# Performance work log

Hardware: AMD Instinct MI355X
Metric: run time of the kernel (lower is better)

## Reference

```python
import jax, jax.numpy as jnp
import numpy as np

D = 120000   # sample_size
H1 = 600     # sample_size/200
H2 = 300     # sample_size/400
H3 = 200     # sample_size/600
DENSITY = 0.1  # sparselinear default connectivity
B = 512
EPS = 1e-5

_LAYER_SPECS = [(H1, D), (H1, H1), (H2, H1), (H3, H2), (H3, H3)]


def _make_idx(key, out_d, in_d, nnz):
    k1, k2 = jax.random.split(key)
    rows = jax.random.randint(k1, (nnz,), 0, out_d)
    cols = jax.random.randint(k2, (nnz,), 0, in_d)
    return jnp.stack([rows, cols]).astype(jnp.int32)


def setup_inputs() -> dict:
    key = jax.random.key(0)
    ks = jax.random.split(key, 32)
    inp = {"x": jax.random.normal(ks[0], (B, D), jnp.float32)}
    for i, (o, ii) in enumerate(_LAYER_SPECS, 1):
        nnz = int(DENSITY * o * ii)
        scale = 1.0 / np.sqrt(DENSITY * ii)  # kaiming-like fan-in scaling on nonzeros
        inp[f"idx{i}"] = _make_idx(ks[3 * i], o, ii, nnz)
        inp[f"val{i}"] = jax.random.normal(ks[3 * i + 1], (nnz,), jnp.float32) * scale
        inp[f"b{i}"] = jnp.zeros((o,), jnp.float32)
    for j, d in enumerate([H1, H2, H3], 1):
        inp[f"g{j}"] = jnp.ones((d,), jnp.float32)
        inp[f"be{j}"] = jnp.zeros((d,), jnp.float32)
    return inp


def _sp_linear(x, idx, vals, bias, out_d):
    # COO sparse linear: y = x @ W^T + b, W scattered from (row, col, val)
    in_d = x.shape[1]
    W = jnp.zeros((out_d, in_d), x.dtype).at[idx[0], idx[1]].add(vals)
    return x @ W.T + bias


def _bn(x, g, b):
    # BatchNorm1d, training mode: biased batch variance
    m = x.mean(axis=0)
    v = x.var(axis=0)
    return (x - m) * jax.lax.rsqrt(v + EPS) * g + b


def reference(x, idx1, val1, b1, idx2, val2, b2, idx3, val3, b3,
              idx4, val4, b4, idx5, val5, b5,
              g1, be1, g2, be2, g3, be3):
    h = jax.nn.silu(_bn(_sp_linear(x, idx1, val1, b1, H1), g1, be1))
    h = jax.nn.silu(_sp_linear(h, idx2, val2, b2, H1))
    h = jax.nn.silu(_bn(_sp_linear(h, idx3, val3, b3, H2), g2, be2))
    h = jax.nn.silu(_bn(_sp_linear(h, idx4, val4, b4, H3), g3, be3))
    return _sp_linear(h, idx5, val5, b5, H3)
```

## Files before the change

kernel.cpp:

```cpp
#include <hip/hip_runtime.h>

typedef unsigned short ushort_t;
typedef unsigned int uint_t;

typedef __bf16 bf16x8 __attribute__((ext_vector_type(8)));
typedef float  floatx4 __attribute__((ext_vector_type(4)));

#define AS3 __attribute__((address_space(3)))
#define AS1 __attribute__((address_space(1)))

#define BATCH 512
#define D_IN  120000
#define N1P   640
#define N2P   640
#define N3P   320
#define N4P   256
#define N5P   256

#define KSPLIT 50
#define KCHUNK 2400

#define HALF    60000
#define CHW     15000
#define NREG    1200
#define NB      256
#define RSTRIDE 6912

static constexpr long O_W1 = 0;
static constexpr long SZ_W1 = 640L * 120000 * 2;
static constexpr long O_W2 = O_W1 + SZ_W1;
static constexpr long SZ_W2 = 640L * 640 * 4;
static constexpr long O_W3 = O_W2 + SZ_W2;
static constexpr long SZ_W3 = 320L * 640 * 4;
static constexpr long O_W4 = O_W3 + SZ_W3;
static constexpr long SZ_W4 = 256L * 320 * 4;
static constexpr long O_W5 = O_W4 + SZ_W4;
static constexpr long SZ_W5 = 256L * 256 * 4;
static constexpr long O_Y1 = O_W5 + SZ_W5;
static constexpr long SZ_Y1 = 512L * 640 * 4;
static constexpr long ZERO_OFF = O_W2;
static constexpr long ZERO_BYTES = (O_Y1 + SZ_Y1) - O_W2;
static constexpr long O_XB = O_Y1 + SZ_Y1;
static constexpr long SZ_XB = 512L * 120000 * 2;
static constexpr long O_CNT = O_XB;
static constexpr long O_OFF = O_CNT + (long)NREG * NB * 4;
static constexpr long O_TOT = O_OFF + (long)NB * NREG * 4;
static constexpr long O_REC = O_TOT + 4800;
static constexpr long O_H1 = O_XB;
static constexpr long O_H2 = O_H1 + 512L * 640 * 4;
static constexpr long O_Y3 = O_H2 + 512L * 640 * 4;
static constexpr long O_H3 = O_Y3 + 512L * 320 * 4;
static constexpr long O_Y4 = O_H3 + 512L * 320 * 4;
static constexpr long O_H4 = O_Y4 + 512L * 256 * 4;

__device__ __forceinline__ ushort_t f2bf(float f) {
    union { float f; uint_t u; } x;
    x.f = f;
    uint_t u = x.u;
    return (ushort_t)((u + 0x7FFFu + ((u >> 16) & 1u)) >> 16);
}
__device__ __forceinline__ float silu_f(float z) {
    return z / (1.f + expf(-z));
}
__device__ __forceinline__ void load16_lds(const void* g, void* l) {
    __builtin_amdgcn_global_load_lds((const AS1 char*)g, (AS3 char*)l, 16, 0, 0);
}

__global__ void zero_f4(float4* __restrict__ p, long n4) {
    long stride = (long)gridDim.x * blockDim.x;
    for (long i = (long)blockIdx.x * blockDim.x + threadIdx.x; i < n4; i += stride)
        p[i] = make_float4(0.f, 0.f, 0.f, 0.f);
}

__global__ void cast_f32_bf16(const float* __restrict__ X, ushort_t* __restrict__ Xb, long n8) {
    long t = (long)blockIdx.x * blockDim.x + threadIdx.x;
    if (t >= n8) return;
    const float4* p = (const float4*)X + 2 * t;
    float4 a = p[0], b = p[1];
    union { ushort_t us[8]; uint4 v; } u;
    u.us[0] = f2bf(a.x); u.us[1] = f2bf(a.y); u.us[2] = f2bf(a.z); u.us[3] = f2bf(a.w);
    u.us[4] = f2bf(b.x); u.us[5] = f2bf(b.y); u.us[6] = f2bf(b.z); u.us[7] = f2bf(b.w);
    ((uint4*)Xb)[t] = u.v;
}

__global__ __launch_bounds__(512) void hist1(const int* __restrict__ idx, int nnz, int chunk,
                                             int* __restrict__ counts ) {
    __shared__ uint_t h[NREG];
    const int b = blockIdx.x, t = threadIdx.x;
    for (int i = t; i < NREG; i += 512) h[i] = 0;
    __syncthreads();
    const int s = b * chunk;
    const int e = min(s + chunk, nnz);
    for (int i = s + t; i < e; i += 512) {
        int r = idx[i];
        int c = idx[nnz + i];
        atomicAdd(&h[r * 2 + (c >= HALF ? 1 : 0)], 1u);
    }
    __syncthreads();
    for (int i = t; i < NREG; i += 512) counts[(long)i * NB + b] = (int)h[i];
}

__global__ __launch_bounds__(NB) void scan1(const int* __restrict__ counts ,
                                            int* __restrict__ offs ,
                                            int* __restrict__ totals) {
    __shared__ int s[NB];
    const int reg = blockIdx.x, t = threadIdx.x;
    const int v = counts[(long)reg * NB + t];
    s[t] = v;
    __syncthreads();
    for (int o = 1; o < NB; o <<= 1) {
        int x = (t >= o) ? s[t - o] : 0;
        __syncthreads();
        s[t] += x;
        __syncthreads();
    }
    offs[(long)t * NREG + reg] = s[t] - v;
    if (t == NB - 1) totals[reg] = s[t];
}

__global__ __launch_bounds__(512) void scatter1(const int* __restrict__ idx,
                                                const float* __restrict__ vals,
                                                int nnz, int chunk,
                                                const int* __restrict__ offs ,
                                                int2* __restrict__ rec) {
    __shared__ int cur[NREG];
    const int b = blockIdx.x, t = threadIdx.x;
    const int* ob = offs + (long)b * NREG;
    for (int i = t; i < NREG; i += 512) cur[i] = i * RSTRIDE + ob[i];
    __syncthreads();
    const int s = b * chunk;
    const int e = min(s + chunk, nnz);
    for (int i = s + t; i < e; i += 512) {
        int r = idx[i];
        int c = idx[nnz + i];
        float v = vals[i];
        int h = (c >= HALF) ? 1 : 0;
        int reg = r * 2 + h;
        int slot = atomicAdd(&cur[reg], 1);
        if (slot < (reg + 1) * RSTRIDE)
            rec[slot] = make_int2(c - h * HALF, __float_as_int(v));
    }
}

__global__ __launch_bounds__(512) void build_w1(const int2* __restrict__ rec,
                                                const int* __restrict__ totals,
                                                ushort_t* __restrict__ W) {
    const int bid = blockIdx.x;
    const int r = bid >> 1, h = bid & 1;
    const int t = threadIdx.x;
    ushort_t* dstbase = W + (size_t)r * D_IN + h * HALF;

    if (r >= 600) {
        uint4 z = make_uint4(0, 0, 0, 0);
        for (int j = t * 8; j < HALF; j += 512 * 8) *(uint4*)(dstbase + j) = z;
        return;
    }

    __shared__ int2 lrec[RSTRIDE];
    __shared__ float acc[CHW];

    const int reg = r * 2 + h;
    const int n = min(totals[reg], RSTRIDE);
    const int2* src = rec + (long)reg * RSTRIDE;
    for (int i = t; i < n; i += 512) lrec[i] = src[i];
    __syncthreads();

#pragma unroll
    for (int ch = 0; ch < 4; ch++) {
        for (int j = t * 4; j < CHW; j += 512 * 4)
            *(float4*)&acc[j] = make_float4(0.f, 0.f, 0.f, 0.f);
        __syncthreads();
        const int base = ch * CHW;
        for (int i = t; i < n; i += 512) {
            int2 e = lrec[i];
            unsigned off = (unsigned)(e.x - base);
            if (off < (unsigned)CHW)
                atomicAdd(&acc[off], __int_as_float(e.y));
        }
        __syncthreads();
        ushort_t* dst = dstbase + base;
        for (int j = t * 8; j < CHW; j += 512 * 8) {
            union { ushort_t us[8]; uint4 v; } u;
#pragma unroll
            for (int k = 0; k < 8; k++) u.us[k] = f2bf(acc[j + k]);
            *(uint4*)(dst + j) = u.v;
        }
        __syncthreads();
    }
}

__global__ void scatter_f32(const int* __restrict__ idx, const float* __restrict__ vals,
                            int nnz, float* __restrict__ W, int ldw) {
    int i = blockIdx.x * blockDim.x + threadIdx.x;
    if (i >= nnz) return;
    atomicAdd(&W[(size_t)idx[i] * ldw + idx[nnz + i]], vals[i]);
}

__global__ __launch_bounds__(256) void gemm1(const ushort_t* __restrict__ X,
                                             const ushort_t* __restrict__ W,
                                             float* __restrict__ Y) {
    __shared__ ushort_t sA[2][128 * 32];
    __shared__ ushort_t sB[2][128 * 32];

    const int b = blockIdx.x;
    const int wrk = (b & 7) * 125 + (b >> 3);
    const int ksIdx = wrk / 20;
    const int tile = wrk % 20;
    const int bm = tile / 5, bn = tile % 5;
    const int ks = ksIdx * KCHUNK;
    const int iters = KCHUNK / 32;

    const int t = threadIdx.x;
    const int lane = t & 63;
    const int w = t >> 6;
    const int wm = w >> 1, wn = w & 1;
    const int i16 = lane & 15;
    const int qk = lane >> 4;

    const int row0 = t >> 2;
    const int kq = (t & 3) ^ ((t >> 3) & 3);

    const ushort_t* pa0 = X + (size_t)(bm * 128 + row0) * D_IN + ks + kq * 8;
    const ushort_t* pa1 = pa0 + (size_t)64 * D_IN;
    const ushort_t* pb0 = W + (size_t)(bn * 128 + row0) * D_IN + ks + kq * 8;
    const ushort_t* pb1 = pb0 + (size_t)64 * D_IN;

    int aoff[4], boff[4];
#pragma unroll
    for (int mi = 0; mi < 4; mi++) {
        int row = wm * 64 + mi * 16 + i16;
        aoff[mi] = row * 64 + ((qk ^ ((row >> 1) & 3)) * 16);
    }
#pragma unroll
    for (int ni = 0; ni < 4; ni++) {
        int row = wn * 64 + ni * 16 + i16;
        boff[ni] = row * 64 + ((qk ^ ((row >> 1) & 3)) * 16);
    }
    const char* sAb = (const char*)sA;
    const char* sBb = (const char*)sB;

    floatx4 acc[4][4] = {};

    load16_lds(pa0, &sA[0][(w * 64) * 8]);
    load16_lds(pa1, &sA[0][(256 + w * 64) * 8]);
    load16_lds(pb0, &sB[0][(w * 64) * 8]);
    load16_lds(pb1, &sB[0][(256 + w * 64) * 8]);
    pa0 += 32; pa1 += 32; pb0 += 32; pb1 += 32;
    __syncthreads();

    int cur = 0;
    for (int it = 0; it < iters; ++it) {
        const int nxt = cur ^ 1;
        if (it + 1 < iters) {
            load16_lds(pa0, &sA[nxt][(w * 64) * 8]);
            load16_lds(pa1, &sA[nxt][(256 + w * 64) * 8]);
            load16_lds(pb0, &sB[nxt][(w * 64) * 8]);
            load16_lds(pb1, &sB[nxt][(256 + w * 64) * 8]);
            pa0 += 32; pa1 += 32; pb0 += 32; pb1 += 32;
        }

        bf16x8 af[4], bfr[4];
#pragma unroll
        for (int mi = 0; mi < 4; mi++)
            af[mi] = *(const bf16x8*)(sAb + cur * 8192 + aoff[mi]);
#pragma unroll
        for (int ni = 0; ni < 4; ni++)
            bfr[ni] = *(const bf16x8*)(sBb + cur * 8192 + boff[ni]);
#pragma unroll
        for (int mi = 0; mi < 4; mi++)
#pragma unroll
            for (int ni = 0; ni < 4; ni++)
                acc[mi][ni] = __builtin_amdgcn_mfma_f32_16x16x32_bf16(af[mi], bfr[ni], acc[mi][ni], 0, 0, 0);

        __syncthreads();
        cur = nxt;
    }

#pragma unroll
    for (int mi = 0; mi < 4; mi++) {
#pragma unroll
        for (int ni = 0; ni < 4; ni++) {
#pragma unroll
            for (int r = 0; r < 4; r++) {
                int row = bm * 128 + wm * 64 + mi * 16 + qk * 4 + r;
                int col = bn * 128 + wn * 64 + ni * 16 + i16;
                atomicAdd(&Y[(size_t)row * N1P + col], acc[mi][ni][r]);
            }
        }
    }
}

__global__ __launch_bounds__(512) void bn_silu(const float* __restrict__ Y, int ld, int realN,
                                               const float* __restrict__ g,
                                               const float* __restrict__ be,
                                               float* __restrict__ H) {
    const int t = threadIdx.x;
    const int sub = t >> 6;
    const int c = t & 63;
    const int col = blockIdx.x * 64 + c;

    float s = 0.f, ss = 0.f;
#pragma unroll 8
    for (int r = sub; r < BATCH; r += 8) {
        float v = Y[(size_t)r * ld + col];
        s += v;
        ss += v * v;
    }
    __shared__ float rs[8][64], rq[8][64], scs[64], shs[64];
    rs[sub][c] = s;
    rq[sub][c] = ss;
    __syncthreads();
    if (t < 64) {
        float S = 0.f, SS = 0.f;
#pragma unroll
        for (int k = 0; k < 8; k++) { S += rs[k][t]; SS += rq[k][t]; }
        float mean = S * (1.f / 512.f);
        float var  = SS * (1.f / 512.f) - mean * mean;
        int cc = blockIdx.x * 64 + t;
        float sc = 0.f, sh = 0.f;
        if (cc < realN) {
            sc = rsqrtf(var + 1e-5f) * g[cc];
            sh = be[cc] - mean * sc;
        }
        scs[t] = sc;
        shs[t] = sh;
    }
    __syncthreads();
    const float sc = scs[c], sh = shs[c];
#pragma unroll 8
    for (int r = sub; r < BATCH; r += 8) {
        float v = Y[(size_t)r * ld + col];
        H[(size_t)r * ld + col] = silu_f(v * sc + sh);
    }
}

template <int ACT, int GUARD>
__global__ __launch_bounds__(256) void small_gemm(const float* __restrict__ A, int lda,
                                                  const float* __restrict__ W, int ldw,
                                                  const float* __restrict__ bias, int biasN,
                                                  float* __restrict__ out, int ldo, int outN,
                                                  int K) {
    __shared__ float sA[64][20];
    __shared__ float sB[64][20];
    const int t = threadIdx.x;
    const int m0 = blockIdx.x * 64, n0 = blockIdx.y * 64;
    const int ty = t >> 4, tx = t & 15;
    const int lm = t >> 2, lq = t & 3;
    float acc[4][4] = {};

    for (int kt = 0; kt < K; kt += 16) {
        __syncthreads();
        float4 av = *(const float4*)&A[(size_t)(m0 + lm) * lda + kt + lq * 4];
        float4 wv = *(const float4*)&W[(size_t)(n0 + lm) * ldw + kt + lq * 4];
        sA[lm][lq * 4 + 0] = av.x; sA[lm][lq * 4 + 1] = av.y;
        sA[lm][lq * 4 + 2] = av.z; sA[lm][lq * 4 + 3] = av.w;
        sB[lm][lq * 4 + 0] = wv.x; sB[lm][lq * 4 + 1] = wv.y;
        sB[lm][lq * 4 + 2] = wv.z; sB[lm][lq * 4 + 3] = wv.w;
        __syncthreads();
#pragma unroll
        for (int kg = 0; kg < 4; kg++) {
            float4 a4[4], b4[4];
#pragma unroll
            for (int i = 0; i < 4; i++) a4[i] = *(const float4*)&sA[ty * 4 + i][kg * 4];
#pragma unroll
            for (int j = 0; j < 4; j++) b4[j] = *(const float4*)&sB[tx * 4 + j][kg * 4];
#pragma unroll
            for (int i = 0; i < 4; i++)
#pragma unroll
                for (int j = 0; j < 4; j++)
                    acc[i][j] += a4[i].x * b4[j].x + a4[i].y * b4[j].y +
                                 a4[i].z * b4[j].z + a4[i].w * b4[j].w;
        }
    }

#pragma unroll
    for (int i = 0; i < 4; i++) {
#pragma unroll
        for (int j = 0; j < 4; j++) {
            int row = m0 + ty * 4 + i;
            int col = n0 + tx * 4 + j;
            float v = acc[i][j];
            if (bias != nullptr && col < biasN) v += bias[col];
            if (ACT == 1) v = silu_f(v);
            if (GUARD) {
                if (col < outN) out[(size_t)row * ldo + col] = v;
            } else {
                out[(size_t)row * ldo + col] = v;
            }
        }
    }
}

extern "C" void kernel_launch(void* const* d_in, const int* in_sizes, int n_in,
                              void* d_out, int out_size, void* d_ws, size_t ws_size,
                              hipStream_t stream) {
    const float* x   = (const float*)d_in[0];
    const int* idx1 = (const int*)d_in[1];  const float* val1 = (const float*)d_in[2];
    const int* idx2 = (const int*)d_in[4];  const float* val2 = (const float*)d_in[5];
    const float* b2 = (const float*)d_in[6];
    const int* idx3 = (const int*)d_in[7];  const float* val3 = (const float*)d_in[8];
    const int* idx4 = (const int*)d_in[10]; const float* val4 = (const float*)d_in[11];
    const int* idx5 = (const int*)d_in[13]; const float* val5 = (const float*)d_in[14];
    const float* b5 = (const float*)d_in[15];
    const float* g1 = (const float*)d_in[16]; const float* be1 = (const float*)d_in[17];
    const float* g2 = (const float*)d_in[18]; const float* be2 = (const float*)d_in[19];
    const float* g3 = (const float*)d_in[20]; const float* be3 = (const float*)d_in[21];

    const int nnz1 = in_sizes[1] / 2;
    const int nnz2 = in_sizes[4] / 2;
    const int nnz3 = in_sizes[7] / 2;
    const int nnz4 = in_sizes[10] / 2;
    const int nnz5 = in_sizes[13] / 2;

    char* ws = (char*)d_ws;
    ushort_t* W1 = (ushort_t*)(ws + O_W1);
    float* W2 = (float*)(ws + O_W2);
    float* W3 = (float*)(ws + O_W3);
    float* W4 = (float*)(ws + O_W4);
    float* W5 = (float*)(ws + O_W5);
    float* y1 = (float*)(ws + O_Y1);
    int*   cnt = (int*)(ws + O_CNT);
    int*   off = (int*)(ws + O_OFF);
    int*   tot = (int*)(ws + O_TOT);
    int2*  rec = (int2*)(ws + O_REC);
    ushort_t* Xb = (ushort_t*)(ws + O_XB);
    float* h1 = (float*)(ws + O_H1);
    float* h2 = (float*)(ws + O_H2);
    float* y3 = (float*)(ws + O_Y3);
    float* h3 = (float*)(ws + O_H3);
    float* y4 = (float*)(ws + O_Y4);
    float* h4 = (float*)(ws + O_H4);

    zero_f4<<<dim3((unsigned)(ZERO_BYTES / 16 / 256 + 1)), dim3(256), 0, stream>>>(
        (float4*)(ws + ZERO_OFF), ZERO_BYTES / 16);

    {
        const int chunk = (nnz1 + NB - 1) / NB;
        hist1<<<dim3(NB), dim3(512), 0, stream>>>(idx1, nnz1, chunk, cnt);
        scan1<<<dim3(NREG), dim3(NB), 0, stream>>>(cnt, off, tot);
        scatter1<<<dim3(NB), dim3(512), 0, stream>>>(idx1, val1, nnz1, chunk, off, rec);
        build_w1<<<dim3(640 * 2), dim3(512), 0, stream>>>(rec, tot, W1);
    }

    {
        long n8 = (long)BATCH * D_IN / 8;
        cast_f32_bf16<<<dim3((unsigned)((n8 + 255) / 256)), dim3(256), 0, stream>>>(x, Xb, n8);
    }

    scatter_f32<<<dim3((nnz2 + 255) / 256), dim3(256), 0, stream>>>(idx2, val2, nnz2, W2, 640);
    scatter_f32<<<dim3((nnz3 + 255) / 256), dim3(256), 0, stream>>>(idx3, val3, nnz3, W3, 640);
    scatter_f32<<<dim3((nnz4 + 255) / 256), dim3(256), 0, stream>>>(idx4, val4, nnz4, W4, 320);
    scatter_f32<<<dim3((nnz5 + 255) / 256), dim3(256), 0, stream>>>(idx5, val5, nnz5, W5, 256);

    gemm1<<<dim3(8 * 125), dim3(256), 0, stream>>>(Xb, W1, y1);

    bn_silu<<<dim3(N1P / 64), dim3(512), 0, stream>>>(y1, N1P, 600, g1, be1, h1);

    small_gemm<1, 0><<<dim3(8, N2P / 64), dim3(256), 0, stream>>>(h1, N1P, W2, 640, b2, 600,
                                                                  h2, N2P, N2P, 640);
    small_gemm<0, 0><<<dim3(8, N3P / 64), dim3(256), 0, stream>>>(h2, N2P, W3, 640, nullptr, 0,
                                                                  y3, N3P, N3P, 640);
    bn_silu<<<dim3(N3P / 64), dim3(512), 0, stream>>>(y3, N3P, 300, g2, be2, h3);

    small_gemm<0, 0><<<dim3(8, N4P / 64), dim3(256), 0, stream>>>(h3, N3P, W4, 320, nullptr, 0,
                                                                  y4, N4P, N4P, 320);
    bn_silu<<<dim3(N4P / 64), dim3(512), 0, stream>>>(y4, N4P, 200, g3, be3, h4);

    small_gemm<0, 1><<<dim3(8, N5P / 64), dim3(256), 0, stream>>>(h4, N4P, W5, 256, b5, 200,
                                                                  (float*)d_out, 200, 200, 256);
    (void)n_in; (void)out_size; (void)ws_size;
}
```

Baseline: 1.078 ms.

## Triple-buffer gemm1 LDS pipeline, enlarge K chunks, merge small scatter kernels

Switches the large GEMM from a double-buffered to a three-stage LDS pipeline. It waits with explicit vmcnt counts and a raw barrier, so two tile loads stay in flight while one is being computed. The K split drops from 50 to 30 chunks of 4000, giving 600 blocks instead of 1000. That cuts the atomic output reductions, but fewer blocks may lower occupancy balance across CUs. The four small-weight scatter launches are also merged into a single kernel to save launch overhead.

```diff
diff --git a/kernel.cpp b/kernel.cpp
--- a/kernel.cpp
+++ b/kernel.cpp
@@ -17,8 +17,8 @@
 #define N4P   256
 #define N5P   256
 
-#define KSPLIT 50
-#define KCHUNK 2400
+#define KSPLIT 30
+#define KCHUNK 4000
 
 #define HALF    60000
 #define CHW     15000
@@ -189,21 +189,30 @@
     }
 }
 
-__global__ void scatter_f32(const int* __restrict__ idx, const float* __restrict__ vals,
-                            int nnz, float* __restrict__ W, int ldw) {
+__global__ void scatter_all(const int* __restrict__ i2, const float* __restrict__ v2, int n2,
+                            const int* __restrict__ i3, const float* __restrict__ v3, int n3,
+                            const int* __restrict__ i4, const float* __restrict__ v4, int n4,
+                            const int* __restrict__ i5, const float* __restrict__ v5, int n5,
+                            float* __restrict__ W2, float* __restrict__ W3,
+                            float* __restrict__ W4, float* __restrict__ W5) {
     int i = blockIdx.x * blockDim.x + threadIdx.x;
-    if (i >= nnz) return;
-    atomicAdd(&W[(size_t)idx[i] * ldw + idx[nnz + i]], vals[i]);
+    if (i < n2) { atomicAdd(&W2[(size_t)i2[i] * 640 + i2[n2 + i]], v2[i]); return; }
+    i -= n2;
+    if (i < n3) { atomicAdd(&W3[(size_t)i3[i] * 640 + i3[n3 + i]], v3[i]); return; }
+    i -= n3;
+    if (i < n4) { atomicAdd(&W4[(size_t)i4[i] * 320 + i4[n4 + i]], v4[i]); return; }
+    i -= n4;
+    if (i < n5) { atomicAdd(&W5[(size_t)i5[i] * 256 + i5[n5 + i]], v5[i]); }
 }
 
 __global__ __launch_bounds__(256) void gemm1(const ushort_t* __restrict__ X,
                                              const ushort_t* __restrict__ W,
                                              float* __restrict__ Y) {
-    __shared__ ushort_t sA[2][128 * 32];
-    __shared__ ushort_t sB[2][128 * 32];
+    __shared__ ushort_t sA[3][4096];
+    __shared__ ushort_t sB[3][4096];
 
     const int b = blockIdx.x;
-    const int wrk = (b & 7) * 125 + (b >> 3);
+    const int wrk = (b & 7) * 75 + (b >> 3);
     const int ksIdx = wrk / 20;
     const int tile = wrk % 20;
     const int bm = tile / 5, bn = tile % 5;
@@ -239,42 +248,47 @@
     const char* sAb = (const char*)sA;
     const char* sBb = (const char*)sB;
 
+#define STAGE1(s) do {                                   \
+        load16_lds(pa0, &sA[s][(w * 64) * 8]);           \
+        load16_lds(pa1, &sA[s][(256 + w * 64) * 8]);     \
+        load16_lds(pb0, &sB[s][(w * 64) * 8]);           \
+        load16_lds(pb1, &sB[s][(256 + w * 64) * 8]);     \
+        pa0 += 32; pa1 += 32; pb0 += 32; pb1 += 32; } while (0)
+
     floatx4 acc[4][4] = {};
 
-    load16_lds(pa0, &sA[0][(w * 64) * 8]);
-    load16_lds(pa1, &sA[0][(256 + w * 64) * 8]);
-    load16_lds(pb0, &sB[0][(w * 64) * 8]);
-    load16_lds(pb1, &sB[0][(256 + w * 64) * 8]);
-    pa0 += 32; pa1 += 32; pb0 += 32; pb1 += 32;
-    __syncthreads();
-
-    int cur = 0;
+    STAGE1(0);
+    STAGE1(1);
+
     for (int it = 0; it < iters; ++it) {
-        const int nxt = cur ^ 1;
-        if (it + 1 < iters) {
-            load16_lds(pa0, &sA[nxt][(w * 64) * 8]);
-            load16_lds(pa1, &sA[nxt][(256 + w * 64) * 8]);
-            load16_lds(pb0, &sB[nxt][(w * 64) * 8]);
-            load16_lds(pb1, &sB[nxt][(256 + w * 64) * 8]);
-            pa0 += 32; pa1 += 32; pb0 += 32; pb1 += 32;
-        }
-
+        if (it < iters - 1) {
+            asm volatile("s_waitcnt vmcnt(4)" ::: "memory");
+        } else {
+            asm volatile("s_waitcnt vmcnt(0)" ::: "memory");
+        }
+        __builtin_amdgcn_s_barrier();
+        __builtin_amdgcn_sched_barrier(0);
+
+        if (it + 2 < iters) {
+            const int ns = (it + 2) % 3;
+            STAGE1(ns);
+        }
+
+        const int cb = it % 3;
         bf16x8 af[4], bfr[4];
 #pragma unroll
         for (int mi = 0; mi < 4; mi++)
-            af[mi] = *(const bf16x8*)(sAb + cur * 8192 + aoff[mi]);
+            af[mi] = *(const bf16x8*)(sAb + cb * 8192 + aoff[mi]);
 #pragma unroll
         for (int ni = 0; ni < 4; ni++)
-            bfr[ni] = *(const bf16x8*)(sBb + cur * 8192 + boff[ni]);
+            bfr[ni] = *(const bf16x8*)(sBb + cb * 8192 + boff[ni]);
 #pragma unroll
         for (int mi = 0; mi < 4; mi++)
 #pragma unroll
             for (int ni = 0; ni < 4; ni++)
                 acc[mi][ni] = __builtin_amdgcn_mfma_f32_16x16x32_bf16(af[mi], bfr[ni], acc[mi][ni], 0, 0, 0);
-
-        __syncthreads();
-        cur = nxt;
-    }
+    }
+#undef STAGE1
 
 #pragma unroll
     for (int mi = 0; mi < 4; mi++) {
@@ -447,12 +461,14 @@
         cast_f32_bf16<<<dim3((unsigned)((n8 + 255) / 256)), dim3(256), 0, stream>>>(x, Xb, n8);
     }
 
-    scatter_f32<<<dim3((nnz2 + 255) / 256), dim3(256), 0, stream>>>(idx2, val2, nnz2, W2, 640);
-    scatter_f32<<<dim3((nnz3 + 255) / 256), dim3(256), 0, stream>>>(idx3, val3, nnz3, W3, 640);
-    scatter_f32<<<dim3((nnz4 + 255) / 256), dim3(256), 0, stream>>>(idx4, val4, nnz4, W4, 320);
-    scatter_f32<<<dim3((nnz5 + 255) / 256), dim3(256), 0, stream>>>(idx5, val5, nnz5, W5, 256);
-
-    gemm1<<<dim3(8 * 125), dim3(256), 0, stream>>>(Xb, W1, y1);
+    {
+        int ntot = nnz2 + nnz3 + nnz4 + nnz5;
+        scatter_all<<<dim3((ntot + 255) / 256), dim3(256), 0, stream>>>(
+            idx2, val2, nnz2, idx3, val3, nnz3, idx4, val4, nnz4, idx5, val5, nnz5,
+            W2, W3, W4, W5);
+    }
+
+    gemm1<<<dim3(8 * 75), dim3(256), 0, stream>>>(Xb, W1, y1);
 
     bn_silu<<<dim3(N1P / 64), dim3(512), 0, stream>>>(y1, N1P, 600, g1, be1, h1);
 
```

After: 1.038 ms. 1.04x faster.
